# Kernel tuning notes

Hardware: AMD Instinct MI355X
Metric: run time of the kernel (lower is better)

The kernel has to match this reference:

```python
import jax, jax.numpy as jnp
import numpy as np

B, L, K, H = 256, 256, 128, 256


def setup_inputs() -> dict:
    key = jax.random.key(0)
    ks = jax.random.split(key, 24)

    def u(k, shape, fan):
        s = 1.0 / np.sqrt(fan)
        return jax.random.uniform(k, shape, minval=-s, maxval=s, dtype=jnp.float32)

    x = jax.random.normal(ks[0], (B, L, K), jnp.float32)
    mask = (jax.random.uniform(ks[1], (B, L, K)) < 0.7).astype(jnp.float32)
    record_num = jax.random.randint(ks[2], (B,), L // 2, L + 1)
    ts = jnp.cumsum(jax.random.uniform(ks[3], (B, L), minval=0.1, maxval=1.0, dtype=jnp.float32), axis=1)
    time_stamp = ts * (jnp.arange(L)[None, :] < record_num[:, None]).astype(jnp.float32)

    return {
        "x": x,
        "mask": mask,
        "time_stamp": time_stamp,
        # TemporalDecay h: W [H,K], stdv = 1/sqrt(out)=1/sqrt(H)
        "W_gh": u(ks[4], (H, K), H), "b_gh": u(ks[5], (H,), H),
        # TemporalDecay x (diag): W [K,K], stdv = 1/sqrt(K)
        "W_gx": u(ks[6], (K, K), K), "b_gx": u(ks[7], (K,), K),
        # hist_reg: Linear(H -> K), stdv = 1/sqrt(H)
        "W_hist": u(ks[8], (K, H), H), "b_hist": u(ks[9], (K,), H),
        "W_feat": u(ks[10], (K, K), K), "b_feat": u(ks[11], (K,), K),
        # weight_combine: Linear(2K -> K), stdv = 1/sqrt(2K)
        "W_comb": u(ks[12], (K, 2 * K), 2 * K), "b_comb": u(ks[13], (K,), 2 * K),
        # GRUCell(2K -> H): uniform 1/sqrt(H)
        "W_ih": u(ks[14], (3 * H, 2 * K), H), "W_hh": u(ks[15], (3 * H, H), H),
        "b_ih": u(ks[16], (3 * H,), H), "b_hh": u(ks[17], (3 * H,), H),
        # out: Linear(H -> 1)
        "W_out": u(ks[18], (1, H), H), "b_out": u(ks[19], (1,), H),
        "record_num": record_num,
        "direct": 0,
    }


def _forward(x, mask, time_stamp, W_gh, b_gh, W_gx, b_gx, W_hist, b_hist,
             W_feat, b_feat, W_comb, b_comb, W_ih, W_hh, b_ih, b_hh,
             W_out, b_out, record_num):
    Bs, Ls, Ks = x.shape
    Hs = W_gh.shape[0]
    eye = jnp.eye(Ks, dtype=x.dtype)
    W_gx_m = W_gx * eye                 # diag temporal decay
    W_feat_m = W_feat * (1.0 - eye)

    # --- deltas (gen_aux_data): d[0]=1; d[t] = |ts[t]-ts[t-1]| + (1-m[t])*d[t-1] ---
    gaps = jnp.abs(jnp.diff(time_stamp, axis=1))          # [B, L-1]
    mask_t = jnp.swapaxes(mask, 0, 1)                     # [L, B, K]

    def dstep(prev, inp):
        gap, m = inp                                      # [B], [B,K]
        d = gap[:, None] + (1.0 - m) * prev
        return d, d

    d0 = jnp.ones((Bs, Ks), x.dtype)
    _, drest = jax.lax.scan(dstep, d0, (gaps.T, mask_t[1:]))
    deltas = jnp.concatenate([d0[None], drest], axis=0)   # [L, B, K]
    valid = (jnp.arange(Ls)[:, None] < record_num[None, :])  # break at record_num
    deltas = jnp.where(valid[:, :, None], deltas, 0.0)

    evals = (time_stamp != 0).astype(x.dtype)             # [B, L]

    x_t = jnp.swapaxes(x, 0, 1)                           # [L, B, K]
    e_t = evals.T                                         # [L, B]

    def step(carry, inp):
        h, xloss = carry
        xt, mt, dt, et = inp                              # [B,K],[B,K],[B,K],[B]
        e_m = et[:, None]
        gamma_h = jnp.exp(-jax.nn.relu(dt @ W_gh.T + b_gh))   # [B,H]
        gamma_x = jnp.exp(-jax.nn.relu(dt @ W_gx_m.T + b_gx)) # [B,K]
        h_prev = h
        h = h * gamma_h
        x_h = h @ W_hist.T + b_hist
        msum = jnp.sum(mt) + 1e-5
        xloss = xloss + jnp.sum(jnp.abs(xt - x_h) * mt) / msum
        x_c = mt * xt + (1.0 - mt) * x_h
        z_h = x_c @ W_feat_m.T + b_feat
        xloss = xloss + jnp.sum(jnp.abs(xt - z_h) * mt * e_m) / msum
        alpha = jnp.concatenate([gamma_x, mt], axis=1) @ W_comb.T + b_comb
        c_h = alpha * z_h + (1.0 - alpha) * x_h
        xloss = xloss + jnp.sum(jnp.abs(xt - c_h) * mt * e_m) / msum
        c_c = mt * xt + (1.0 - mt) * c_h
        inputs = jnp.concatenate([c_c, mt], axis=1)           # [B, 2K]
        gi = inputs @ W_ih.T + b_ih                           # [B, 3H]
        gh = h @ W_hh.T + b_hh
        ir, iz, ig = jnp.split(gi, 3, axis=1)
        hr, hz, hg = jnp.split(gh, 3, axis=1)
        r = jax.nn.sigmoid(ir + hr)
        z = jax.nn.sigmoid(iz + hz)
        n = jnp.tanh(ig + r * hg)
        h_new = (1.0 - z) * n + z * h
        h_new = h_new * e_m + (1.0 - e_m) * h_prev            # freeze h past record
        return (h_new, xloss), c_c * e_m

    h0 = jnp.zeros((Bs, Hs), x.dtype)
    (h_fin, x_loss), imps = jax.lax.scan(step, (h0, jnp.float32(0.0)), (x_t, mask_t, deltas, e_t))
    imputations = jnp.swapaxes(imps, 0, 1)                # [B, L, K]
    predictions = jax.nn.sigmoid(h_fin @ W_out.T + b_out) # [B, 1]
    return imputations, x_loss, predictions


def reference(x, mask, time_stamp, W_gh, b_gh, W_gx, b_gx, W_hist, b_hist,
              W_feat, b_feat, W_comb, b_comb, W_ih, W_hh, b_ih, b_hh,
              W_out, b_out, record_num, direct):
    return _forward(x, mask, time_stamp, W_gh, b_gh, W_gx, b_gx, W_hist, b_hist,
                    W_feat, b_feat, W_comb, b_comb, W_ih, W_hh, b_ih, b_hh,
                    W_out, b_out, record_num)
```

## Files before the change

### kernel.cpp

```cpp
#include <hip/hip_runtime.h>
#include <math.h>

#define BT 256
#define LT 256
#define KT 128
#define HT 256
#define LOSS_IDX ((size_t)BT*LT*KT)
#define PRED_IDX (LOSS_IDX + 1)
#define LDP 1280
#define GH0 0
#define AL0 256
#define GI0 384
#define ZP0 1152

typedef _Float16 h2 __attribute__((ext_vector_type(2)));
typedef _Float16 f16x8 __attribute__((ext_vector_type(8)));
typedef float f32x4 __attribute__((ext_vector_type(4)));

__device__ __forceinline__ float fd2(h2 a, h2 b, float c){
#if __has_builtin(__builtin_amdgcn_fdot2)
  return __builtin_amdgcn_fdot2(a, b, c, false);
#else
  return c + (float)a[0]*(float)b[0] + (float)a[1]*(float)b[1];
#endif
}
__device__ __forceinline__ h2 lo2(f16x8 v){ return __builtin_shufflevector(v,v,0,1); }
__device__ __forceinline__ h2 p1v(f16x8 v){ return __builtin_shufflevector(v,v,2,3); }
__device__ __forceinline__ h2 p2v(f16x8 v){ return __builtin_shufflevector(v,v,4,5); }
__device__ __forceinline__ h2 p3v(f16x8 v){ return __builtin_shufflevector(v,v,6,7); }
__device__ __forceinline__ float sigf(float v){ return 1.0f/(1.0f + __expf(-v)); }
__device__ __forceinline__ float tanh_fast(float v){
  float a = fminf(fabsf(v), 15.0f);
  float e2 = __expf(2.0f*a);
  float r = (e2 - 1.0f)/(e2 + 1.0f);
  return copysignf(r, v);
}
__device__ __forceinline__ float f16bits(unsigned u, int hi){
  union { unsigned short s; _Float16 h; } c;
  c.s = (unsigned short)(hi ? (u >> 16) : (u & 0xffff));
  return (float)c.h;
}

__global__ void pack_cast(const float* __restrict__ src, _Float16* __restrict__ dst,
                          int J, int Kd, int diag, int total){
  int idx = blockIdx.x*256 + threadIdx.x;
  if (idx >= total) return;
  float v = src[idx];
  if (diag && (idx / Kd) == (idx % Kd)) v = 0.0f;
  dst[idx] = (_Float16)v;
}
__global__ void pack_rowchunks(const float* __restrict__ src, _Float16* __restrict__ dst,
                               int J, int K, int total){
  int idx = blockIdx.x*256 + threadIdx.x;
  if (idx >= total) return;
  int j = idx % J, c = idx / J;
  #pragma unroll
  for (int e = 0; e < 8; ++e)
    dst[(size_t)idx*8 + e] = (_Float16)src[(size_t)j*K + c*8 + e];
}
__global__ void pack_col(const float* __restrict__ src, _Float16* __restrict__ dst,
                         int J, int Kc, int ld, int diag, int total){
  int idx = blockIdx.x*256 + threadIdx.x;
  if (idx >= total) return;
  int j = idx % J, k = idx / J;
  float v = src[(size_t)j*ld + k];
  if (diag && j == k) v = 0.0f;
  dst[idx] = (_Float16)v;
}
__global__ void pack_colpair(const float* __restrict__ src, _Float16* __restrict__ dst,
                             int total){
  int idx = blockIdx.x*256 + threadIdx.x;
  if (idx >= total) return;
  int k = idx / 384, m = idx % 384;
  dst[(size_t)2*idx]     = (_Float16)src[(size_t)m*(2*KT) + k];
  dst[(size_t)2*idx + 1] = (_Float16)src[(size_t)(m + 384)*(2*KT) + k];
}

__global__ __launch_bounds__(128) void scan_kernel(
    const float* __restrict__ x, const float* __restrict__ mask, const float* __restrict__ ts,
    const float* __restrict__ W_gx, const float* __restrict__ b_gx,
    const int* __restrict__ record_num,
    _Float16* __restrict__ deltas, _Float16* __restrict__ Agx, _Float16* __restrict__ U)
{
  int b = blockIdx.x, k = threadIdx.x;
  int rn = record_num[b];
  float gxd = W_gx[(size_t)k*KT + k];
  float bgx = b_gx[k];
  float d = 1.0f, tsp = 0.0f;
  for (int t0 = 0; t0 < LT; t0 += 8){
    float xv[8], mv[8], tsv[8];
    #pragma unroll
    for (int u = 0; u < 8; ++u){
      size_t off = ((size_t)b*LT + t0 + u)*KT + k;
      xv[u] = x[off]; mv[u] = mask[off];
      tsv[u] = ts[(size_t)b*LT + t0 + u];
    }
    #pragma unroll
    for (int u = 0; u < 8; ++u){
      int t = t0 + u;
      if (t > 0){
        float gap = fabsf(tsv[u] - (u ? tsv[u-1] : tsp));
        d = gap + (1.0f - mv[u])*d;
      }
      float e = (t < rn) ? 1.0f : 0.0f;
      float dev = d * e;
      size_t row = (size_t)b*LT + t;
      deltas[row*KT + k] = (_Float16)dev;
      float gx = __expf(-fmaxf(fmaf(dev, gxd, bgx), 0.0f));
      Agx[row*2*KT + k]      = (_Float16)gx;
      Agx[row*2*KT + KT + k] = (_Float16)mv[u];
      U[row*2*KT + k]        = (_Float16)(mv[u]*xv[u]);
      U[row*2*KT + KT + k]   = (_Float16)mv[u];
    }
    tsp = tsv[7];
  }
}

__global__ void msum_kernel(const float* __restrict__ mask, float* __restrict__ msumInv){
  __shared__ float red[256];
  int t = blockIdx.x;
  float acc = 0.0f;
  for (int i = threadIdx.x; i < BT*KT; i += 256){
    int b = i >> 7, k = i & 127;
    acc += mask[((size_t)b*LT + t)*KT + k];
  }
  red[threadIdx.x] = acc; __syncthreads();
  for (int s = 128; s > 0; s >>= 1){
    if (threadIdx.x < s) red[threadIdx.x] += red[threadIdx.x + s];
    __syncthreads();
  }
  if (threadIdx.x == 0) msumInv[t] = 1.0f/(red[0] + 1e-5f);
}

__global__ __launch_bounds__(256) void gemm_f16(
    const _Float16* __restrict__ A, long ldA, int K,
    const _Float16* __restrict__ B, long ldB,
    _Float16* __restrict__ C, long colofs,
    const float* __restrict__ bias, int op)
{
  const int w = threadIdx.x >> 6, lane = threadIdx.x & 63;
  const int ml = lane & 15, quad = lane >> 4;
  const long m0 = (long)blockIdx.x*64 + w*16;
  const long nb0 = (long)blockIdx.y*64;
  f32x4 acc[4] = {{0,0,0,0},{0,0,0,0},{0,0,0,0},{0,0,0,0}};
  for (int kc = 0; kc < K; kc += 32){
    f16x8 a = *(const f16x8*)(A + (m0 + ml)*ldA + kc + quad*8);
    #pragma unroll
    for (int nt = 0; nt < 4; ++nt){
      f16x8 bfr = *(const f16x8*)(B + (nb0 + nt*16 + ml)*ldB + kc + quad*8);
      acc[nt] = __builtin_amdgcn_mfma_f32_16x16x32_f16(a, bfr, acc[nt], 0, 0, 0);
    }
  }
  #pragma unroll
  for (int nt = 0; nt < 4; ++nt){
    long col = nb0 + nt*16 + ml;
    float bv = (op >= 1) ? bias[col] : 0.0f;
    #pragma unroll
    for (int r = 0; r < 4; ++r){
      float v = acc[nt][r];
      if (op >= 1) v += bv;
      if (op == 2) v = __expf(-fmaxf(v, 0.0f));
      long row = m0 + quad*4 + r;
      C[row*LDP + colofs + col] = (_Float16)v;
    }
  }
}

#define NTS 1024

struct __align__(16) SeqS {
  f16x8 whist_l[32*128];
  h2 wfcp[128*64];
  float h[HT];
  float hs[HT];
  alignas(16) _Float16 hsh[HT];
  float gh[3*HT];
  float gi[3*HT];
  float v3[KT];
  float v5[KT];
  int lidx[KT];
  unsigned gam[128];
  unsigned pbd[2][512];
  float xb[2][KT], mb[2][KT];
  float bhist[KT], bfeat[KT];
  float bhh[3*HT];
  float wout[HT];
  float minv[LT];
};

__global__ __launch_bounds__(NTS) void rits_seq(
    const float* __restrict__ x, const float* __restrict__ mask,
    const int* __restrict__ record_num, const float* __restrict__ msumInv,
    const _Float16* __restrict__ P,
    const f16x8* __restrict__ Whh_p, const f16x8* __restrict__ Whist_p,
    const _Float16* __restrict__ Wfc, const _Float16* __restrict__ Wihc,
    const float* __restrict__ b_hist, const float* __restrict__ b_feat,
    const float* __restrict__ b_hh,
    const float* __restrict__ W_out, const float* __restrict__ b_out,
    float* __restrict__ out)
{
  __shared__ SeqS s;
  const int tid = threadIdx.x;
  const int b = blockIdx.x;
  const int rn = record_num[b];
  const unsigned* __restrict__ Pd = (const unsigned*)P + (size_t)b*LT*(LDP/2);

  for (int i = tid; i < 32*128; i += NTS) s.whist_l[i] = Whist_p[i];
  for (int i = tid; i < 128*64; i += NTS){
    int k = i >> 6, l = i & 63;
    h2 w; w[0] = Wfc[k*128 + l]; w[1] = Wfc[k*128 + 64 + l];
    s.wfcp[i] = w;
  }
  if (tid < HT){ s.h[tid] = 0.0f; s.hs[tid] = 0.0f; s.hsh[tid] = (_Float16)0.0f;
                 s.wout[tid] = W_out[tid]; }
  if (tid < KT){ s.bhist[tid] = b_hist[tid]; s.bfeat[tid] = b_feat[tid]; }
  if (tid >= 256 && tid < 256 + 3*HT) s.bhh[tid - 256] = b_hh[tid - 256];
  if (tid >= 64 && tid < 576) s.pbd[0][tid - 64] = Pd[128 + (tid - 64)];
  if (tid >= 576 && tid < 704){
    int k = tid - 576;
    s.xb[0][k] = x[((size_t)b*LT)*KT + k];
    s.mb[0][k] = mask[((size_t)b*LT)*KT + k];
  }
  if (tid >= 704 && tid < 960) s.minv[tid - 704] = msumInv[tid - 704];
  __syncthreads();

  float loss = 0.0f;

  for (int t = 0; t < LT; ++t){
    const int cur = t & 1, nxt = cur ^ 1;
    const int last = (t == LT - 1);

    if (tid < 64){
      const int j0 = tid, j1 = tid + 64;
      const float inv = s.minv[t];
      float mv0 = s.mb[cur][j0], mv1 = s.mb[cur][j1];
      float xv0 = s.xb[cur][j0], xv1 = s.xb[cur][j1];
      bool miss0 = (mv0 == 0.0f), miss1 = (mv1 == 0.0f);
      unsigned long long bal0 = __ballot(miss0);
      unsigned long long bal1 = __ballot(miss1);
      unsigned long long ltm = (1ull << tid) - 1ull;
      int cA = __popcll(bal0);
      int c0 = cA + __popcll(bal1);
      int pos0 = __popcll(bal0 & ltm);
      int pos1 = cA + __popcll(bal1 & ltm);
      if (miss0) s.lidx[pos0] = j0;
      if (miss1) s.lidx[pos1] = j1;
      const f16x8* hp = (const f16x8*)s.hsh;
      float A0=0.f,A1=0.f,A2=0.f,A3=0.f,B0=0.f,B1=0.f,B2=0.f,B3=0.f;
      #pragma unroll 8
      for (int c = 0; c < 32; ++c){
        f16x8 av = hp[c];
        f16x8 w0 = s.whist_l[c*128 + j0];
        f16x8 w1 = s.whist_l[c*128 + j1];
        A0 = fd2(lo2(w0), lo2(av), A0); A1 = fd2(p1v(w0), p1v(av), A1);
        A2 = fd2(p2v(w0), p2v(av), A2); A3 = fd2(p3v(w0), p3v(av), A3);
        B0 = fd2(lo2(w1), lo2(av), B0); B1 = fd2(p1v(w1), p1v(av), B1);
        B2 = fd2(p2v(w1), p2v(av), B2); B3 = fd2(p3v(w1), p3v(av), B3);
      }
      float xh0 = (A0+A1)+(A2+A3) + s.bhist[j0];
      float xh1 = (B0+B1)+(B2+B3) + s.bhist[j1];
      loss += (fabsf(xv0 - xh0)*mv0 + fabsf(xv1 - xh1)*mv1) * inv;
      if (miss0) s.v3[pos0] = xh0;
      if (miss1) s.v3[pos1] = xh1;
      float za0=0.f, za1=0.f, zb0=0.f, zb1=0.f;
      {
        int i = 0;
        for (; i + 1 < c0; i += 2){
          int l0 = s.lidx[i], l1 = s.lidx[i + 1];
          float v0 = s.v3[i], v1 = s.v3[i + 1];
          h2 wa = s.wfcp[l0*64 + tid];
          h2 wb = s.wfcp[l1*64 + tid];
          za0 += v0*(float)wa[0]; za1 += v0*(float)wa[1];
          zb0 += v1*(float)wb[0]; zb1 += v1*(float)wb[1];
        }
        if (i < c0){
          int l0 = s.lidx[i]; float v0 = s.v3[i];
          h2 wa = s.wfcp[l0*64 + tid];
          za0 += v0*(float)wa[0]; za1 += v0*(float)wa[1];
        }
      }
      float z0 = f16bits(s.pbd[cur][448 + (j0 >> 1)], j0 & 1) + s.bfeat[j0] + za0 + zb0;
      float z1 = f16bits(s.pbd[cur][448 + (j1 >> 1)], j1 & 1) + s.bfeat[j1] + za1 + zb1;
      float al0 = f16bits(s.pbd[cur][j0 >> 1], j0 & 1);
      float al1 = f16bits(s.pbd[cur][j1 >> 1], j1 & 1);
      float e = (t < rn) ? 1.0f : 0.0f;
      float ch0 = al0*z0 + (1.0f - al0)*xh0;
      float ch1 = al1*z1 + (1.0f - al1)*xh1;
      loss += ((fabsf(xv0 - z0) + fabsf(xv0 - ch0))*mv0
             + (fabsf(xv1 - z1) + fabsf(xv1 - ch1))*mv1) * e * inv;
      float cc0 = mv0*xv0 + (1.0f - mv0)*ch0;
      float cc1 = mv1*xv1 + (1.0f - mv1)*ch1;
      out[((size_t)b*LT + t)*KT + j0] = cc0 * e;
      out[((size_t)b*LT + t)*KT + j1] = cc1 * e;
      if (miss0) s.v5[pos0] = ch0;
      if (miss1) s.v5[pos1] = ch1;
      float g[12];
      #pragma unroll
      for (int u = 0; u < 6; ++u){
        int m = tid + 64*u;
        g[u]     = f16bits(s.pbd[cur][64 + (m >> 1)], m & 1);
        int m2 = m + 384;
        g[6 + u] = f16bits(s.pbd[cur][64 + (m2 >> 1)], m2 & 1);
      }
      for (int i = 0; i < c0; ++i){
        float vv = s.v5[i];
        const h2* wr = (const h2*)(Wihc + (size_t)s.lidx[i]*768);
        #pragma unroll
        for (int u = 0; u < 6; ++u){
          h2 w = wr[tid + 64*u];
          g[u]     += vv*(float)w[0];
          g[6 + u] += vv*(float)w[1];
        }
      }
      #pragma unroll
      for (int u = 0; u < 6; ++u){
        s.gi[tid + 64*u]       = g[u];
        s.gi[384 + tid + 64*u] = g[6 + u];
      }
    } else if (tid < 832) {
      const int gj = tid - 64;
      const f16x8* hp = (const f16x8*)s.hsh;
      float a0=0.f, a1=0.f, a2=0.f, a3=0.f;
      #pragma unroll 8
      for (int c = 0; c < 32; ++c){
        f16x8 w = Whh_p[c*768 + gj];
        f16x8 av = hp[c];
        a0 = fd2(lo2(w), lo2(av), a0);
        a1 = fd2(p1v(w), p1v(av), a1);
        a2 = fd2(p2v(w), p2v(av), a2);
        a3 = fd2(p3v(w), p3v(av), a3);
      }
      s.gh[gj] = (a0 + a1) + (a2 + a3);
    } else {
      if (!last){
        int pf = tid - 832;
        const unsigned* Pn = Pd + (size_t)(t + 1)*(LDP/2);
        if (pf < 128){
          s.gam[pf] = Pn[pf];
          #pragma unroll
          for (int u = 0; u < 4; ++u)
            s.pbd[nxt][u*128 + pf] = Pn[128 + u*128 + pf];
        } else {
          int k2 = pf - 128;
          const float2* xp = (const float2*)(x + ((size_t)b*LT + t + 1)*KT);
          const float2* mp = (const float2*)(mask + ((size_t)b*LT + t + 1)*KT);
          float2 xv = xp[k2], mv = mp[k2];
          s.xb[nxt][2*k2] = xv.x;   s.xb[nxt][2*k2 + 1] = xv.y;
          s.mb[nxt][2*k2] = mv.x;   s.mb[nxt][2*k2 + 1] = mv.y;
        }
      }
    }
    __syncthreads();

    if (tid < HT){
      const int j = tid;
      float ir = s.gi[j], iz = s.gi[HT + j], ig = s.gi[2*HT + j];
      float hr = s.gh[j] + s.bhh[j];
      float hz = s.gh[HT + j] + s.bhh[HT + j];
      float hg = s.gh[2*HT + j] + s.bhh[2*HT + j];
      float r = sigf(ir + hr);
      float zg = sigf(iz + hz);
      float n = tanh_fast(ig + r*hg);
      float hn = (1.0f - zg)*n + zg*s.hs[j];
      float he = (t < rn) ? hn : s.h[j];
      s.h[j] = he;
      if (!last){
        float gn = f16bits(s.gam[j >> 1], j & 1);
        float hsn = he * gn;
        s.hs[j] = hsn;
        s.hsh[j] = (_Float16)hsn;
      }
    }
    __syncthreads();
  }

  if (tid < 64){
    #pragma unroll
    for (int off = 32; off; off >>= 1) loss += __shfl_down(loss, off);
    if (tid == 0) atomicAdd(&out[LOSS_IDX], loss);
  }

  if (tid < HT) s.gi[tid] = s.h[tid] * s.wout[tid];
  __syncthreads();
  for (int st2 = 128; st2 > 0; st2 >>= 1){
    if (tid < st2) s.gi[tid] += s.gi[tid + st2];
    __syncthreads();
  }
  if (tid == 0) out[PRED_IDX + b] = sigf(s.gi[0] + b_out[0]);
}

extern "C" void kernel_launch(void* const* d_in, const int* in_sizes, int n_in,
                              void* d_out, int out_size, void* d_ws, size_t ws_size,
                              hipStream_t stream){
  const float* x      = (const float*)d_in[0];
  const float* mask   = (const float*)d_in[1];
  const float* ts     = (const float*)d_in[2];
  const float* W_gh   = (const float*)d_in[3];
  const float* b_gh   = (const float*)d_in[4];
  const float* W_gx   = (const float*)d_in[5];
  const float* b_gx   = (const float*)d_in[6];
  const float* W_hist = (const float*)d_in[7];
  const float* b_hist = (const float*)d_in[8];
  const float* W_feat = (const float*)d_in[9];
  const float* b_feat = (const float*)d_in[10];
  const float* W_comb = (const float*)d_in[11];
  const float* b_comb = (const float*)d_in[12];
  const float* W_ih   = (const float*)d_in[13];
  const float* W_hh   = (const float*)d_in[14];
  const float* b_ih   = (const float*)d_in[15];
  const float* b_hh   = (const float*)d_in[16];
  const float* W_out  = (const float*)d_in[17];
  const float* b_out  = (const float*)d_in[18];
  const int*   rn     = (const int*)d_in[19];
  float* out = (float*)d_out;
  char* ws = (char*)d_ws;

  size_t off = 0;
  auto alloc = [&](size_t bytes) -> char* {
    char* p = ws + off;
    off += (bytes + 255) & ~(size_t)255;
    return p;
  };
  _Float16* P      = (_Float16*)alloc((size_t)BT*LT*LDP*2);
  _Float16* deltas = (_Float16*)alloc((size_t)BT*LT*KT*2);
  _Float16* Agx    = (_Float16*)alloc((size_t)BT*LT*2*KT*2);
  _Float16* U      = (_Float16*)alloc((size_t)BT*LT*2*KT*2);
  _Float16* WghF   = (_Float16*)alloc(HT*KT*2);
  _Float16* WcombF = (_Float16*)alloc(KT*2*KT*2);
  _Float16* WihF   = (_Float16*)alloc(3*HT*2*KT*2);
  _Float16* WfeatF = (_Float16*)alloc(KT*KT*2);
  _Float16* Whh_p  = (_Float16*)alloc(3*HT*HT*2);
  _Float16* Whist_p= (_Float16*)alloc(KT*HT*2);
  _Float16* Wfc    = (_Float16*)alloc(KT*KT*2);
  _Float16* Wihc   = (_Float16*)alloc(KT*3*HT*2);
  float* msumInv   = (float*)alloc(LT*4);

  auto grid1 = [](int n){ return dim3((n + 255)/256); };
  pack_cast<<<grid1(HT*KT), 256, 0, stream>>>(W_gh, WghF, HT, KT, 0, HT*KT);
  pack_cast<<<grid1(KT*2*KT), 256, 0, stream>>>(W_comb, WcombF, KT, 2*KT, 0, KT*2*KT);
  pack_cast<<<grid1(3*HT*2*KT), 256, 0, stream>>>(W_ih, WihF, 3*HT, 2*KT, 0, 3*HT*2*KT);
  pack_cast<<<grid1(KT*KT), 256, 0, stream>>>(W_feat, WfeatF, KT, KT, 1, KT*KT);
  pack_rowchunks<<<grid1(3*HT*(HT/8)), 256, 0, stream>>>(W_hh, Whh_p, 3*HT, HT, 3*HT*(HT/8));
  pack_rowchunks<<<grid1(KT*(HT/8)), 256, 0, stream>>>(W_hist, Whist_p, KT, HT, KT*(HT/8));
  pack_col<<<grid1(KT*KT), 256, 0, stream>>>(W_feat, Wfc, KT, KT, KT, 1, KT*KT);
  pack_colpair<<<grid1(KT*384), 256, 0, stream>>>(W_ih, Wihc, KT*384);

  scan_kernel<<<dim3(BT), dim3(KT), 0, stream>>>(x, mask, ts, W_gx, b_gx, rn, deltas, Agx, U);
  msum_kernel<<<dim3(LT), dim3(256), 0, stream>>>(mask, msumInv);

  const int MR = BT*LT;
  gemm_f16<<<dim3(MR/64, HT/64), 256, 0, stream>>>(deltas, KT, KT, WghF, KT, P, GH0, b_gh, 2);
  gemm_f16<<<dim3(MR/64, KT/64), 256, 0, stream>>>(Agx, 2*KT, 2*KT, WcombF, 2*KT, P, AL0, b_comb, 1);
  gemm_f16<<<dim3(MR/64, 3*HT/64), 256, 0, stream>>>(U, 2*KT, 2*KT, WihF, 2*KT, P, GI0, b_ih, 1);
  gemm_f16<<<dim3(MR/64, KT/64), 256, 0, stream>>>(U, 2*KT, KT, WfeatF, KT, P, ZP0, (const float*)nullptr, 0);

  hipMemsetAsync((void*)(out + LOSS_IDX), 0, sizeof(float), stream);

  rits_seq<<<dim3(BT), dim3(NTS), 0, stream>>>(x, mask, rn, msumInv, P,
      (const f16x8*)Whh_p, (const f16x8*)Whist_p, Wfc, Wihc,
      b_hist, b_feat, b_hh, W_out, b_out, out);
}
```

Measured before the change: 2.493 ms.

## Quantize W_hh to per-row scaled FP8 and repack W_ih columns for wide loads

The recurrent W_hh matvec in the sequential kernel now reads FP8 E4M3 weights with per-row scales and converts them with the hardware cvt_pk_f32_fp8 instruction, halving the weight bytes streamed each timestep. Each block also starts the chunk loop at a different offset, so concurrent blocks hit different cache lines. The missing-feature W_ih column update is repacked so each thread pulls its 12 weights with two 16-byte loads instead of six scattered 4-byte loads. FP8 weights cut precision in the GRU hidden update and may push accuracy past tolerance over the 256 recurrent steps.

```diff
diff --git a/kernel.cpp b/kernel.cpp
--- a/kernel.cpp
+++ b/kernel.cpp
@@ -16,6 +16,13 @@
 typedef _Float16 h2 __attribute__((ext_vector_type(2)));
 typedef _Float16 f16x8 __attribute__((ext_vector_type(8)));
 typedef float f32x4 __attribute__((ext_vector_type(4)));
+typedef float f32x2 __attribute__((ext_vector_type(2)));
+
+#if defined(__has_builtin)
+#if __has_builtin(__builtin_amdgcn_cvt_pk_f32_fp8)
+#define HAVE_CVT_FP8 1
+#endif
+#endif
 
 __device__ __forceinline__ float fd2(h2 a, h2 b, float c){
 #if __has_builtin(__builtin_amdgcn_fdot2)
@@ -41,6 +48,26 @@
   return (float)c.h;
 }
 
+__device__ unsigned char f32_to_e4m3(float v){
+  unsigned u = __float_as_uint(v);
+  unsigned s = (u >> 24) & 0x80;
+  float a = fabsf(v);
+  if (a == 0.0f) return (unsigned char)s;
+  if (a >= 448.0f) return (unsigned char)(s | 0x7E);
+  int e; float m = frexpf(a, &e);
+  int E = e - 1;
+  if (E < -6){
+    float q = a * 512.0f;
+    int qi = (int)(q + 0.5f);
+    if (qi > 7) return (unsigned char)(s | 0x08);
+    return (unsigned char)(s | qi);
+  }
+  float mf = (m * 2.0f - 1.0f) * 8.0f;
+  int mi = (int)(mf + 0.5f);
+  if (mi == 8){ mi = 0; E += 1; if (E > 8) return (unsigned char)(s | 0x7E); }
+  return (unsigned char)(s | ((E + 7) << 3) | mi);
+}
+
 __global__ void pack_cast(const float* __restrict__ src, _Float16* __restrict__ dst,
                           int J, int Kd, int diag, int total){
   int idx = blockIdx.x*256 + threadIdx.x;
@@ -67,13 +94,30 @@
   if (diag && j == k) v = 0.0f;
   dst[idx] = (_Float16)v;
 }
-__global__ void pack_colpair(const float* __restrict__ src, _Float16* __restrict__ dst,
-                             int total){
+__global__ void pack_whh8(const float* __restrict__ src, unsigned char* __restrict__ dst,
+                          float* __restrict__ rinv){
+  int j = blockIdx.x*256 + threadIdx.x;
+  if (j >= 768) return;
+  float amax = 0.0f;
+  for (int k = 0; k < 256; ++k) amax = fmaxf(amax, fabsf(src[(size_t)j*256 + k]));
+  float scale = (amax > 0.0f) ? (240.0f / amax) : 1.0f;
+  rinv[j] = (amax > 0.0f) ? (amax / 240.0f) : 0.0f;
+  for (int c = 0; c < 16; ++c)
+    for (int e = 0; e < 16; ++e)
+      dst[((size_t)c*768 + j)*16 + e] = f32_to_e4m3(src[(size_t)j*256 + c*16 + e] * scale);
+}
+__global__ void pack_wih4(const float* __restrict__ src, _Float16* __restrict__ dst, int total){
   int idx = blockIdx.x*256 + threadIdx.x;
   if (idx >= total) return;
-  int k = idx / 384, m = idx % 384;
-  dst[(size_t)2*idx]     = (_Float16)src[(size_t)m*(2*KT) + k];
-  dst[(size_t)2*idx + 1] = (_Float16)src[(size_t)(m + 384)*(2*KT) + k];
+  int k = idx >> 6, u = idx & 63;
+  size_t base = ((size_t)k*64 + u)*16;
+  #pragma unroll
+  for (int v = 0; v < 6; ++v){
+    dst[base + 2*v]     = (_Float16)src[(size_t)(u + 64*v)*256 + k];
+    dst[base + 2*v + 1] = (_Float16)src[(size_t)(u + 64*v + 384)*256 + k];
+  }
+  dst[base + 12] = (_Float16)0.0f; dst[base + 13] = (_Float16)0.0f;
+  dst[base + 14] = (_Float16)0.0f; dst[base + 15] = (_Float16)0.0f;
 }
 
 __global__ __launch_bounds__(128) void scan_kernel(
@@ -176,6 +220,7 @@
   alignas(16) _Float16 hsh[HT];
   float gh[3*HT];
   float gi[3*HT];
+  float rinv_l[3*HT];
   float v3[KT];
   float v5[KT];
   int lidx[KT];
@@ -192,8 +237,10 @@
     const float* __restrict__ x, const float* __restrict__ mask,
     const int* __restrict__ record_num, const float* __restrict__ msumInv,
     const _Float16* __restrict__ P,
-    const f16x8* __restrict__ Whh_p, const f16x8* __restrict__ Whist_p,
-    const _Float16* __restrict__ Wfc, const _Float16* __restrict__ Wihc,
+    const uint4* __restrict__ Whh8, const float* __restrict__ rinv,
+    const f16x8* __restrict__ Whh_p,
+    const f16x8* __restrict__ Whist_p,
+    const _Float16* __restrict__ Wfc, const _Float16* __restrict__ Wih4,
     const float* __restrict__ b_hist, const float* __restrict__ b_feat,
     const float* __restrict__ b_hh,
     const float* __restrict__ W_out, const float* __restrict__ b_out,
@@ -215,6 +262,7 @@
                  s.wout[tid] = W_out[tid]; }
   if (tid < KT){ s.bhist[tid] = b_hist[tid]; s.bfeat[tid] = b_feat[tid]; }
   if (tid >= 256 && tid < 256 + 3*HT) s.bhh[tid - 256] = b_hh[tid - 256];
+  for (int i = tid; i < 3*HT; i += NTS) s.rinv_l[i] = rinv[i];
   if (tid >= 64 && tid < 576) s.pbd[0][tid - 64] = Pd[128 + (tid - 64)];
   if (tid >= 576 && tid < 704){
     int k = tid - 576;
@@ -225,6 +273,11 @@
   __syncthreads();
 
   float loss = 0.0f;
+#ifdef HAVE_CVT_FP8
+  const int cstart = (b * 5) & 15;
+#else
+  const int cstart = (b * 5) & 31;
+#endif
 
   for (int t = 0; t < LT; ++t){
     const int cur = t & 1, nxt = cur ^ 1;
@@ -302,15 +355,17 @@
         int m2 = m + 384;
         g[6 + u] = f16bits(s.pbd[cur][64 + (m2 >> 1)], m2 & 1);
       }
+      const uint4* W4 = (const uint4*)Wih4;
       for (int i = 0; i < c0; ++i){
         float vv = s.v5[i];
-        const h2* wr = (const h2*)(Wihc + (size_t)s.lidx[i]*768);
-        #pragma unroll
-        for (int u = 0; u < 6; ++u){
-          h2 w = wr[tid + 64*u];
-          g[u]     += vv*(float)w[0];
-          g[6 + u] += vv*(float)w[1];
-        }
+        const uint4* Wp = W4 + ((size_t)s.lidx[i]*64 + tid)*2;
+        uint4 wa = Wp[0], wb = Wp[1];
+        g[0] += vv*f16bits(wa.x,0); g[6]  += vv*f16bits(wa.x,1);
+        g[1] += vv*f16bits(wa.y,0); g[7]  += vv*f16bits(wa.y,1);
+        g[2] += vv*f16bits(wa.z,0); g[8]  += vv*f16bits(wa.z,1);
+        g[3] += vv*f16bits(wa.w,0); g[9]  += vv*f16bits(wa.w,1);
+        g[4] += vv*f16bits(wb.x,0); g[10] += vv*f16bits(wb.x,1);
+        g[5] += vv*f16bits(wb.y,0); g[11] += vv*f16bits(wb.y,1);
       }
       #pragma unroll
       for (int u = 0; u < 6; ++u){
@@ -319,10 +374,30 @@
       }
     } else if (tid < 832) {
       const int gj = tid - 64;
+      float a0=0.f, a1=0.f, a2=0.f, a3=0.f;
+#ifdef HAVE_CVT_FP8
+      #pragma unroll
+      for (int it = 0; it < 16; ++it){
+        int c = (cstart + it) & 15;
+        uint4 w = Whh8[(size_t)c*768 + gj];
+        const float4* hv = (const float4*)&s.hs[c*16];
+        float4 h0 = hv[0], h1 = hv[1], h2f = hv[2], h3 = hv[3];
+        f32x2 p;
+        p = __builtin_amdgcn_cvt_pk_f32_fp8(w.x, false); a0 = fmaf(p[0], h0.x, a0); a1 = fmaf(p[1], h0.y, a1);
+        p = __builtin_amdgcn_cvt_pk_f32_fp8(w.x, true);  a2 = fmaf(p[0], h0.z, a2); a3 = fmaf(p[1], h0.w, a3);
+        p = __builtin_amdgcn_cvt_pk_f32_fp8(w.y, false); a0 = fmaf(p[0], h1.x, a0); a1 = fmaf(p[1], h1.y, a1);
+        p = __builtin_amdgcn_cvt_pk_f32_fp8(w.y, true);  a2 = fmaf(p[0], h1.z, a2); a3 = fmaf(p[1], h1.w, a3);
+        p = __builtin_amdgcn_cvt_pk_f32_fp8(w.z, false); a0 = fmaf(p[0], h2f.x, a0); a1 = fmaf(p[1], h2f.y, a1);
+        p = __builtin_amdgcn_cvt_pk_f32_fp8(w.z, true);  a2 = fmaf(p[0], h2f.z, a2); a3 = fmaf(p[1], h2f.w, a3);
+        p = __builtin_amdgcn_cvt_pk_f32_fp8(w.w, false); a0 = fmaf(p[0], h3.x, a0); a1 = fmaf(p[1], h3.y, a1);
+        p = __builtin_amdgcn_cvt_pk_f32_fp8(w.w, true);  a2 = fmaf(p[0], h3.z, a2); a3 = fmaf(p[1], h3.w, a3);
+      }
+      s.gh[gj] = ((a0 + a1) + (a2 + a3)) * s.rinv_l[gj];
+#else
       const f16x8* hp = (const f16x8*)s.hsh;
-      float a0=0.f, a1=0.f, a2=0.f, a3=0.f;
       #pragma unroll 8
-      for (int c = 0; c < 32; ++c){
+      for (int it = 0; it < 32; ++it){
+        int c = (cstart + it) & 31;
         f16x8 w = Whh_p[c*768 + gj];
         f16x8 av = hp[c];
         a0 = fd2(lo2(w), lo2(av), a0);
@@ -331,6 +406,7 @@
         a3 = fd2(p3v(w), p3v(av), a3);
       }
       s.gh[gj] = (a0 + a1) + (a2 + a3);
+#endif
     } else {
       if (!last){
         int pf = tid - 832;
@@ -430,9 +506,11 @@
   _Float16* WihF   = (_Float16*)alloc(3*HT*2*KT*2);
   _Float16* WfeatF = (_Float16*)alloc(KT*KT*2);
   _Float16* Whh_p  = (_Float16*)alloc(3*HT*HT*2);
+  unsigned char* Whh8 = (unsigned char*)alloc(3*HT*HT);
+  float* rinv      = (float*)alloc(3*HT*4);
   _Float16* Whist_p= (_Float16*)alloc(KT*HT*2);
   _Float16* Wfc    = (_Float16*)alloc(KT*KT*2);
-  _Float16* Wihc   = (_Float16*)alloc(KT*3*HT*2);
+  _Float16* Wih4   = (_Float16*)alloc((size_t)KT*64*16*2);
   float* msumInv   = (float*)alloc(LT*4);
 
   auto grid1 = [](int n){ return dim3((n + 255)/256); };
@@ -441,9 +519,10 @@
   pack_cast<<<grid1(3*HT*2*KT), 256, 0, stream>>>(W_ih, WihF, 3*HT, 2*KT, 0, 3*HT*2*KT);
   pack_cast<<<grid1(KT*KT), 256, 0, stream>>>(W_feat, WfeatF, KT, KT, 1, KT*KT);
   pack_rowchunks<<<grid1(3*HT*(HT/8)), 256, 0, stream>>>(W_hh, Whh_p, 3*HT, HT, 3*HT*(HT/8));
+  pack_whh8<<<grid1(3*HT), 256, 0, stream>>>(W_hh, Whh8, rinv);
   pack_rowchunks<<<grid1(KT*(HT/8)), 256, 0, stream>>>(W_hist, Whist_p, KT, HT, KT*(HT/8));
   pack_col<<<grid1(KT*KT), 256, 0, stream>>>(W_feat, Wfc, KT, KT, KT, 1, KT*KT);
-  pack_colpair<<<grid1(KT*384), 256, 0, stream>>>(W_ih, Wihc, KT*384);
+  pack_wih4<<<grid1(KT*64), 256, 0, stream>>>(W_ih, Wih4, KT*64);
 
   scan_kernel<<<dim3(BT), dim3(KT), 0, stream>>>(x, mask, ts, W_gx, b_gx, rn, deltas, Agx, U);
   msum_kernel<<<dim3(LT), dim3(256), 0, stream>>>(mask, msumInv);
@@ -457,6 +536,7 @@
   hipMemsetAsync((void*)(out + LOSS_IDX), 0, sizeof(float), stream);
 
   rits_seq<<<dim3(BT), dim3(NTS), 0, stream>>>(x, mask, rn, msumInv, P,
-      (const f16x8*)Whh_p, (const f16x8*)Whist_p, Wfc, Wihc,
+      (const uint4*)Whh8, rinv, (const f16x8*)Whh_p,
+      (const f16x8*)Whist_p, Wfc, Wih4,
       b_hist, b_feat, b_hh, W_out, b_out, out);
 }
```

New measurement: 3.939 ms. 1.58x slower.
